# Kernel optimization log

Hardware: AMD Instinct MI355X
Metric: run time of the kernel (lower is better)

## Reference

```python
import jax, jax.numpy as jnp
import numpy as np

D_MODEL = 2048
N_HEADS = 16
HEAD_DIM = 128
WINDOW = 256
B, T = 2, 2048
SCALE = float(np.sqrt(HEAD_DIM))


def setup_inputs() -> dict:
    key = jax.random.key(0)
    ks = jax.random.split(key, 5)
    init = 0.02
    x = jax.random.normal(ks[0], (B, T, D_MODEL), dtype=jnp.float32)
    Wq = jax.random.normal(ks[1], (D_MODEL, D_MODEL), dtype=jnp.float32) * init
    Wk = jax.random.normal(ks[2], (D_MODEL, D_MODEL), dtype=jnp.float32) * init
    Wv = jax.random.normal(ks[3], (D_MODEL, D_MODEL), dtype=jnp.float32) * init
    Wo = jax.random.normal(ks[4], (D_MODEL, D_MODEL), dtype=jnp.float32) * init
    return {"x": x, "Wq": Wq, "Wk": Wk, "Wv": Wv, "Wo": Wo}


def _allowed_mask():
    # [H, T, T] bool: global (even) heads -> causal; local (odd) heads -> causal band of WINDOW
    idx = jnp.arange(T)
    causal = idx[None, :] <= idx[:, None]                      # [T, T]
    band = idx[None, :] >= (idx[:, None] - WINDOW + 1)         # [T, T]
    is_global = (jnp.arange(N_HEADS) % 2) == 0                 # [H]
    return causal[None] & (is_global[:, None, None] | band[None])


def reference(x, Wq, Wk, Wv, Wo):
    # projections (nn.Linear: y = x @ W.T), reshape to [B, H, T, D]
    def proj(W):
        return (x @ W.T).reshape(B, T, N_HEADS, HEAD_DIM).transpose(0, 2, 1, 3)

    q, k, v = proj(Wq), proj(Wk), proj(Wv)
    scores = jnp.einsum("bhtd,bhsd->bhts", q, k) / SCALE       # [B, H, T, T]
    allowed = _allowed_mask()                                  # [H, T, T]
    neg_inf = jnp.asarray(-jnp.inf, dtype=scores.dtype)
    scores = jnp.where(allowed[None], scores, neg_inf)
    attn = jax.nn.softmax(scores, axis=-1)
    out = jnp.einsum("bhts,bhsd->bhtd", attn, v)               # [B, H, T, D]
    concat = out.transpose(0, 2, 1, 3).reshape(B, T, N_HEADS * HEAD_DIM)
    return concat @ Wo.T
```

## Files before the change

kernel.cpp:

```cpp
#include <hip/hip_runtime.h>

typedef __attribute__((ext_vector_type(4))) float f32x4;
typedef __attribute__((ext_vector_type(8))) short bf16x8;
typedef __attribute__((ext_vector_type(4))) unsigned short u16x4;
typedef unsigned short u16;

#define MFMA16(a, b, c) __builtin_amdgcn_mfma_f32_16x16x32_bf16((a), (b), (c), 0, 0, 0)

#define T_SEQ 2048
#define DMODEL 2048
#define NHEADS 16
#define HDIM 128
#define WINDOW 256
#define MROWS 4096
#define SC 0.08838834764831845f

__device__ __forceinline__ u16 f2bf(float f) {
  union { float f; unsigned u; } v; v.f = f;
  return (u16)((v.u + 0x7FFFu + ((v.u >> 16) & 1u)) >> 16);
}
__device__ __forceinline__ float bf2f(u16 u) {
  union { unsigned u; float f; } v; v.u = ((unsigned)u) << 16;
  return v.f;
}
__device__ __forceinline__ void gl_lds16(const u16* g, u16* l) {
  __builtin_amdgcn_global_load_lds((const __attribute__((address_space(1))) void*)(g),
                                   (__attribute__((address_space(3))) void*)(l), 16, 0, 0);
}

#define BAR __builtin_amdgcn_s_barrier()
#define FEN asm volatile("" ::: "memory")
#define VMC3 asm volatile("s_waitcnt vmcnt(3)" ::: "memory")
#define VMC2 asm volatile("s_waitcnt vmcnt(2)" ::: "memory")
#define VMC0 asm volatile("s_waitcnt vmcnt(0)" ::: "memory")

__global__ __launch_bounds__(256) void convert_all(const float* __restrict__ x,
                                                   const float* __restrict__ wq,
                                                   const float* __restrict__ wk,
                                                   const float* __restrict__ wv,
                                                   const float* __restrict__ wo,
                                                   u16* __restrict__ dst) {
  const size_t NX = (size_t)MROWS * DMODEL;
  const size_t NW = (size_t)DMODEL * DMODEL;
  const size_t chunks = (NX + 4 * NW) / 8;
  for (size_t ci = (size_t)blockIdx.x * 256 + threadIdx.x; ci < chunks;
       ci += (size_t)gridDim.x * 256) {
    const size_t off = ci * 8;
    const float* src;
    size_t so;
    if (off < NX) { src = x; so = off; }
    else {
      size_t rem = off - NX;
      if (rem < NW) { src = wq; so = rem; }
      else if (rem < 2 * NW) { src = wk; so = rem - NW; }
      else if (rem < 3 * NW) { src = wv; so = rem - 2 * NW; }
      else { src = wo; so = rem - 3 * NW; }
    }
    f32x4 a = *(const f32x4*)&src[so];
    f32x4 b = *(const f32x4*)&src[so + 4];
    bf16x8 o;
#pragma unroll
    for (int j = 0; j < 4; ++j) { o[j] = (short)f2bf(a[j]); o[j + 4] = (short)f2bf(b[j]); }
    *(bf16x8*)&dst[off] = o;
  }
}

__global__ __launch_bounds__(512, 2) void gemm_qkv(const u16* __restrict__ A,
                                                   const u16* __restrict__ W,
                                                   u16* __restrict__ qb,
                                                   u16* __restrict__ kb,
                                                   u16* __restrict__ vb) {
  __shared__ u16 lds[57344];
  const int tid = threadIdx.x, w = tid >> 6, lane = tid & 63;
  const int wm = w >> 2, wn = w & 3;
  const int fr = lane & 15, g = lane >> 4, g4 = g * 4;

  const int xcd = blockIdx.x & 7, bi = blockIdx.x >> 3;
  const int mt = bi >> 2, nt = xcd * 4 + (bi & 3);
  const int m0 = mt * 256, n0 = nt * 192;

  const int xs0 = (g ^ (fr & 7)) * 8;
  const int xs1 = xs0 ^ 32;
  const int aRow = wm * 128 + fr;
  const int bRow = wn * 48 + fr;

  const int sr = tid >> 3;
  const int scc = ((tid & 7) ^ (sr & 7)) * 8;
  const u16* pA0  = A + (size_t)(m0 + sr) * DMODEL + scc;
  const u16* pA1  = A + (size_t)(m0 + 64 + sr) * DMODEL + scc;
  const u16* pB0  = W + (size_t)(n0 + sr) * DMODEL + scc;
  const u16* pB0b = W + (size_t)(n0 + 64 + sr) * DMODEL + scc;
  const u16* pB1  = W + (size_t)(n0 + 128 + sr) * DMODEL + scc;

#define SAH(h, t, c)                                                                   \
  { gl_lds16(pA0 + (size_t)(h) * 128 * DMODEL + (t) * 64,                              \
             &lds[(c) * 16384 + (h) * 8192 + w * 512]);                                \
    gl_lds16(pA1 + (size_t)(h) * 128 * DMODEL + (t) * 64,                              \
             &lds[(c) * 16384 + (h) * 8192 + 4096 + w * 512]); }
#define SBH0(t, c)                                                                     \
  { gl_lds16(pB0 + (size_t)(t) * 64, &lds[32768 + (c) * 12288 + w * 512]);             \
    gl_lds16(pB0b + (size_t)(t) * 64, &lds[32768 + (c) * 12288 + 4096 + w * 512]); }
#define SBH1(t, c)                                                                     \
  { gl_lds16(pB1 + (size_t)(t) * 64, &lds[32768 + (c) * 12288 + 8192 + w * 512]); }

#define RD_AL(c)                                                                       \
  { _Pragma("unroll") for (int m_ = 0; m_ < 4; ++m_) {                                 \
      af[m_][0] = *(const bf16x8*)&lds[(c) * 16384 + (aRow + m_ * 16) * 64 + xs0];     \
      af[m_][1] = *(const bf16x8*)&lds[(c) * 16384 + (aRow + m_ * 16) * 64 + xs1]; } }
#define RD_AH(c)                                                                       \
  { _Pragma("unroll") for (int m_ = 0; m_ < 4; ++m_) {                                 \
      af[m_][0] = *(const bf16x8*)&lds[(c) * 16384 + (aRow + 64 + m_ * 16) * 64 + xs0];\
      af[m_][1] = *(const bf16x8*)&lds[(c) * 16384 + (aRow + 64 + m_ * 16) * 64 + xs1]; } }
#define RD_B(c)                                                                        \
  { _Pragma("unroll") for (int n_ = 0; n_ < 3; ++n_) {                                 \
      bfr[n_][0] = *(const bf16x8*)&lds[32768 + (c) * 12288 + (bRow + n_ * 16) * 64 + xs0]; \
      bfr[n_][1] = *(const bf16x8*)&lds[32768 + (c) * 12288 + (bRow + n_ * 16) * 64 + xs1]; } }

#define MMQ(MB)                                                                        \
  { __builtin_amdgcn_s_setprio(1);                                                    \
    _Pragma("unroll") for (int kc_ = 0; kc_ < 2; ++kc_)                                \
      _Pragma("unroll") for (int m_ = 0; m_ < 4; ++m_)                                 \
        _Pragma("unroll") for (int n_ = 0; n_ < 3; ++n_)                               \
          acc[(MB) + m_][n_] = MFMA16(af[m_][kc_], bfr[n_][kc_], acc[(MB) + m_][n_]);  \
    __builtin_amdgcn_s_setprio(0); }

  bf16x8 af[4][2], bfr[3][2];
  f32x4 acc[8][3];
#pragma unroll
  for (int i = 0; i < 8; ++i)
#pragma unroll
    for (int j = 0; j < 3; ++j) acc[i][j] = (f32x4){0.f, 0.f, 0.f, 0.f};

  SAH(0, 0, 0); SAH(1, 0, 0);
  SBH0(0, 0); SBH1(0, 0);
  SBH0(1, 1); SBH1(1, 1);
  VMC3; BAR;

#pragma unroll 1
  for (int i = 0; i < 15; ++i) {
    const int t0 = 2 * i;
    RD_AL(0); RD_B(0); SAH(0, t0 + 1, 1); SAH(1, t0 + 1, 1);
    FEN; BAR; MMQ(0); FEN; BAR;
    RD_AH(0); SBH0(t0 + 2, 0); SBH1(t0 + 2, 0);
    VMC3; BAR; MMQ(4); FEN; BAR;
    RD_AL(1); RD_B(1); SAH(0, t0 + 2, 0); SAH(1, t0 + 2, 0);
    FEN; BAR; MMQ(0); FEN; BAR;
    RD_AH(1); SBH0(t0 + 3, 1); SBH1(t0 + 3, 1);
    VMC3; BAR; MMQ(4); FEN; BAR;
  }
  RD_AL(0); RD_B(0); SAH(0, 31, 1); SAH(1, 31, 1);
  FEN; BAR; MMQ(0); FEN; BAR;
  RD_AH(0);
  VMC0; BAR; MMQ(4); FEN; BAR;
  RD_AL(1); RD_B(1);
  FEN; BAR; MMQ(0); FEN; BAR;
  RD_AH(1);
  FEN; BAR; MMQ(4);

#pragma unroll
  for (int mi = 0; mi < 8; ++mi)
#pragma unroll
    for (int ni = 0; ni < 3; ++ni) {
      const int row0 = m0 + wm * 128 + mi * 16 + g4;
      const int cg = n0 + wn * 48 + ni * 16 + fr;
      const int bb = row0 >> 11, tl = row0 & 2047;
      if (cg < DMODEL) {
#pragma unroll
        for (int r = 0; r < 4; ++r)
          qb[(size_t)(row0 + r) * DMODEL + cg] = f2bf(acc[mi][ni][r] * SC);
      } else if (cg < 2 * DMODEL) {
        const int cc = cg - DMODEL;
        const int hh = cc >> 7, d = cc & 127;
        const size_t kbase = (size_t)(bb * NHEADS + hh) * T_SEQ * HDIM;
#pragma unroll
        for (int r = 0; r < 4; ++r)
          kb[kbase + (size_t)(tl + r) * HDIM + d] = f2bf(acc[mi][ni][r]);
      } else {
        const int cc = cg - 2 * DMODEL;
        const int hh = cc >> 7, d = cc & 127;
        u16x4 w4;
#pragma unroll
        for (int r = 0; r < 4; ++r) w4[r] = f2bf(acc[mi][ni][r]);
        *(u16x4*)&vb[(size_t)(bb * NHEADS + hh) * T_SEQ * HDIM + (size_t)(tl >> 6) * 8192 +
                     d * 64 + (tl & 63)] = w4;
      }
    }
#undef SAH
#undef SBH0
#undef SBH1
#undef RD_AL
#undef RD_AH
#undef RD_B
#undef MMQ
}

__global__ __launch_bounds__(512, 2) void gemm_out(const u16* __restrict__ A,
                                                   const u16* __restrict__ W0,
                                                   float* __restrict__ outf) {
  __shared__ u16 lds2[49152];
  const int tid = threadIdx.x, w = tid >> 6, lane = tid & 63;
  const int wm = w >> 2, wn = w & 3;
  const int fr = lane & 15, g = lane >> 4, g4 = g * 4;

  const int xcd = blockIdx.x & 7, bi = blockIdx.x >> 3;
  const int mt = bi >> 1, nt = xcd * 2 + (bi & 1);
  const int m0 = mt * 256, n0 = nt * 128;

  const int xs0 = (g ^ (fr & 7)) * 8;
  const int xs1 = xs0 ^ 32;
  const int aRow = wm * 128 + fr;
  const int bRow = wn * 32 + fr;

  const int sr = tid >> 3;
  const int scc = ((tid & 7) ^ (sr & 7)) * 8;
  const u16* pA0  = A + (size_t)(m0 + sr) * DMODEL + scc;
  const u16* pA1  = A + (size_t)(m0 + 64 + sr) * DMODEL + scc;
  const u16* pB0  = W0 + (size_t)(n0 + sr) * DMODEL + scc;
  const u16* pB0b = W0 + (size_t)(n0 + 64 + sr) * DMODEL + scc;

#define S2A(h, t, c)                                                                   \
  { gl_lds16(pA0 + (size_t)(h) * 128 * DMODEL + (t) * 64,                              \
             &lds2[(c) * 16384 + (h) * 8192 + w * 512]);                               \
    gl_lds16(pA1 + (size_t)(h) * 128 * DMODEL + (t) * 64,                              \
             &lds2[(c) * 16384 + (h) * 8192 + 4096 + w * 512]); }
#define S2B(t, c)                                                                      \
  { gl_lds16(pB0 + (size_t)(t) * 64, &lds2[32768 + (c) * 8192 + w * 512]);             \
    gl_lds16(pB0b + (size_t)(t) * 64, &lds2[32768 + (c) * 8192 + 4096 + w * 512]); }

#define R2AL(c)                                                                        \
  { _Pragma("unroll") for (int m_ = 0; m_ < 4; ++m_) {                                 \
      af[m_][0] = *(const bf16x8*)&lds2[(c) * 16384 + (aRow + m_ * 16) * 64 + xs0];    \
      af[m_][1] = *(const bf16x8*)&lds2[(c) * 16384 + (aRow + m_ * 16) * 64 + xs1]; } }
#define R2AH(c)                                                                        \
  { _Pragma("unroll") for (int m_ = 0; m_ < 4; ++m_) {                                 \
      af[m_][0] = *(const bf16x8*)&lds2[(c) * 16384 + (aRow + 64 + m_ * 16) * 64 + xs0]; \
      af[m_][1] = *(const bf16x8*)&lds2[(c) * 16384 + (aRow + 64 + m_ * 16) * 64 + xs1]; } }
#define R2B(c)                                                                         \
  { _Pragma("unroll") for (int n_ = 0; n_ < 2; ++n_) {                                 \
      bfr[n_][0] = *(const bf16x8*)&lds2[32768 + (c) * 8192 + (bRow + n_ * 16) * 64 + xs0]; \
      bfr[n_][1] = *(const bf16x8*)&lds2[32768 + (c) * 8192 + (bRow + n_ * 16) * 64 + xs1]; } }

#define M2(MB)                                                                         \
  { __builtin_amdgcn_s_setprio(1);                                                    \
    _Pragma("unroll") for (int kc_ = 0; kc_ < 2; ++kc_)                                \
      _Pragma("unroll") for (int m_ = 0; m_ < 4; ++m_)                                 \
        _Pragma("unroll") for (int n_ = 0; n_ < 2; ++n_)                               \
          acc[(MB) + m_][n_] = MFMA16(af[m_][kc_], bfr[n_][kc_], acc[(MB) + m_][n_]);  \
    __builtin_amdgcn_s_setprio(0); }

  bf16x8 af[4][2], bfr[2][2];
  f32x4 acc[8][2];
#pragma unroll
  for (int i = 0; i < 8; ++i)
#pragma unroll
    for (int j = 0; j < 2; ++j) acc[i][j] = (f32x4){0.f, 0.f, 0.f, 0.f};

  S2A(0, 0, 0); S2A(1, 0, 0);
  S2B(0, 0);
  S2B(1, 1);
  VMC2; BAR;

#pragma unroll 1
  for (int i = 0; i < 15; ++i) {
    const int t0 = 2 * i;
    R2AL(0); R2B(0); S2A(0, t0 + 1, 1); S2A(1, t0 + 1, 1);
    FEN; BAR; M2(0); FEN; BAR;
    R2AH(0); S2B(t0 + 2, 0);
    VMC2; BAR; M2(4); FEN; BAR;
    R2AL(1); R2B(1); S2A(0, t0 + 2, 0); S2A(1, t0 + 2, 0);
    FEN; BAR; M2(0); FEN; BAR;
    R2AH(1); S2B(t0 + 3, 1);
    VMC2; BAR; M2(4); FEN; BAR;
  }
  R2AL(0); R2B(0); S2A(0, 31, 1); S2A(1, 31, 1);
  FEN; BAR; M2(0); FEN; BAR;
  R2AH(0);
  VMC0; BAR; M2(4); FEN; BAR;
  R2AL(1); R2B(1);
  FEN; BAR; M2(0); FEN; BAR;
  R2AH(1);
  FEN; BAR; M2(4);

#pragma unroll
  for (int mi = 0; mi < 8; ++mi)
#pragma unroll
    for (int ni = 0; ni < 2; ++ni) {
      const int row0 = m0 + wm * 128 + mi * 16 + g4;
      const int c = n0 + wn * 32 + ni * 16 + fr;
#pragma unroll
      for (int r = 0; r < 4; ++r)
        outf[(size_t)(row0 + r) * DMODEL + c] = acc[mi][ni][r];
    }
#undef S2A
#undef S2B
#undef R2AL
#undef R2AH
#undef R2B
#undef M2
}

#define QB 128
#define KVB 64

__global__ __launch_bounds__(512, 4) void attn_kernel(const u16* __restrict__ qb,
                                                      const u16* __restrict__ kb,
                                                      const u16* __restrict__ vb,
                                                      u16* __restrict__ op,
                                                      u16* __restrict__ pO,
                                                      float* __restrict__ pm,
                                                      float* __restrict__ pl) {
  __shared__ u16 lds[40960];

  const int xcdid = blockIdx.x & 7, j = blockIdx.x >> 3;
  const int p = xcdid * 4 + j / 24;
  const int bx = j % 24;
  const int h = p & 15, b = p >> 4;

  const bool isglobal = (h & 1) == 0;
  int qt, klo, khi, part = 0;
  bool partial = false;
  if (isglobal) {
    if (bx < 16) {
      qt = 15 - (bx >> 1);
      part = bx & 1;
      partial = true;
      if (part == 0) { klo = 0; khi = 15; } else { klo = 16; khi = 2 * qt + 1; }
    } else {
      qt = 23 - bx;
      klo = 0; khi = 2 * qt + 1;
    }
  } else {
    if (bx >= 16) return;
    qt = 15 - bx;
    const int lo_ = qt * QB - (WINDOW - 1);
    klo = lo_ > 0 ? (lo_ >> 6) : 0;
    khi = 2 * qt + 1;
  }

  const int tid = threadIdx.x, wave = tid >> 6, lane = tid & 63;
  const int fr = lane & 15, g = lane >> 4, g4 = g * 4;
  const int xk = fr & 7;
  const int q0 = qt * QB;
  const int bh = b * NHEADS + h;
  const size_t basek = (size_t)bh * T_SEQ * HDIM;
  const size_t baseo = (size_t)b * T_SEQ * DMODEL + (size_t)h * HDIM;

  bf16x8 qf[4];
  {
    const int qrow = q0 + wave * 16 + fr;
#pragma unroll
    for (int ds = 0; ds < 4; ++ds)
      qf[ds] = *(const bf16x8*)&qb[(size_t)b * T_SEQ * DMODEL + (size_t)qrow * DMODEL +
                                   (size_t)h * HDIM + ds * 32 + g * 8];
  }

  float mrun = -1e30f, lrun = 0.f;
  f32x4 o[8];
#pragma unroll
  for (int dt = 0; dt < 8; ++dt) o[dt] = (f32x4){0.f, 0.f, 0.f, 0.f};

  const int j0 = wave * 2, j1 = wave * 2 + 1;
  const int gi0 = j0 * 64 + lane, gi1 = j1 * 64 + lane;
  const int kr0 = gi0 >> 4, kc0 = (gi0 & 15) ^ (kr0 & 7);
  const int kr1 = gi1 >> 4, kc1 = (gi1 & 15) ^ (kr1 & 7);
  const u16* pK0 = kb + basek + (size_t)kr0 * HDIM + kc0 * 8;
  const u16* pK1 = kb + basek + (size_t)kr1 * HDIM + kc1 * 8;
  const int d0 = gi0 >> 3, vs0 = (gi0 & 7) ^ (d0 & 7);
  const int d1 = gi1 >> 3, vs1 = (gi1 & 7) ^ (d1 & 7);
  const u16* pV0 = vb + basek + (size_t)d0 * 64 + vs0 * 8;
  const u16* pV1 = vb + basek + (size_t)d1 * 64 + vs1 * 8;

#define STAGE(KT, c)                                                                   \
  { gl_lds16(pK0 + (size_t)(KT) * 8192, &lds[(c) * 8192 + j0 * 512]);                  \
    gl_lds16(pK1 + (size_t)(KT) * 8192, &lds[(c) * 8192 + j1 * 512]);                  \
    gl_lds16(pV0 + (size_t)(KT) * 8192, &lds[16384 + (c) * 8192 + j0 * 512]);          \
    gl_lds16(pV1 + (size_t)(KT) * 8192, &lds[16384 + (c) * 8192 + j1 * 512]); }

  u16* Pw = &lds[32768 + wave * 1024];
  const int qg = q0 + wave * 16 + fr;

  STAGE(klo, klo & 1);
  VMC0; BAR;

  for (int kt = klo; kt <= khi; ++kt) {
    const int c = kt & 1;
    const bool more = kt < khi;
    if (more) STAGE(kt + 1, c ^ 1);
    const u16* Kc = &lds[c * 8192];
    const u16* Vc = &lds[16384 + c * 8192];

    f32x4 s[4];
    __builtin_amdgcn_s_setprio(1);
#pragma unroll
    for (int kk = 0; kk < 4; ++kk) {
      f32x4 a = (f32x4){0.f, 0.f, 0.f, 0.f};
#pragma unroll
      for (int ds = 0; ds < 4; ++ds) {
        const int r = kk * 16 + fr;
        bf16x8 kf = *(const bf16x8*)&Kc[r * 128 + (((ds * 4 + g) ^ xk) << 3)];
        a = MFMA16(kf, qf[ds], a);
      }
      s[kk] = a;
    }
    __builtin_amdgcn_s_setprio(0);

    float sv[16];
    float pmax = -1e30f;
#pragma unroll
    for (int kk = 0; kk < 4; ++kk)
#pragma unroll
      for (int reg = 0; reg < 4; ++reg) {
        const int cg = kt * KVB + kk * 16 + g4 + reg;
        const bool allowed = (cg <= qg) && (isglobal || cg >= qg - (WINDOW - 1));
        const float v = allowed ? s[kk][reg] : -1e30f;
        sv[kk * 4 + reg] = v;
        pmax = fmaxf(pmax, v);
      }
    pmax = fmaxf(pmax, __shfl_xor(pmax, 16, 64));
    pmax = fmaxf(pmax, __shfl_xor(pmax, 32, 64));
    const bool resc = !__all(pmax - mrun <= 8.0f);
    float fac = 1.f;
    if (resc) {
      const float nm = fmaxf(mrun, pmax);
      fac = __expf(mrun - nm);
      mrun = nm;
    }
    float rs = 0.f;
    u16 pb[16];
#pragma unroll
    for (int i = 0; i < 16; ++i) {
      const float p_ = (sv[i] > -5e29f) ? __expf(sv[i] - mrun) : 0.f;
      rs += p_;
      pb[i] = f2bf(p_);
    }
    rs += __shfl_xor(rs, 16, 64);
    rs += __shfl_xor(rs, 32, 64);
    lrun = lrun * fac + rs;

#pragma unroll
    for (int kk = 0; kk < 4; ++kk) {
      u16x4 wv;
      wv[0] = pb[kk * 4]; wv[1] = pb[kk * 4 + 1]; wv[2] = pb[kk * 4 + 2]; wv[3] = pb[kk * 4 + 3];
      *(u16x4*)&Pw[fr * 64 + (((2 * kk + (g >> 1)) ^ xk) << 3) + (g & 1) * 4] = wv;
    }

    if (resc) {
      float ff[4];
#pragma unroll
      for (int r = 0; r < 4; ++r) ff[r] = __shfl(fac, g4 + r, 64);
#pragma unroll
      for (int dt = 0; dt < 8; ++dt)
#pragma unroll
        for (int r = 0; r < 4; ++r) o[dt][r] *= ff[r];
    }

    bf16x8 pf0 = *(const bf16x8*)&Pw[fr * 64 + ((g ^ xk) << 3)];
    bf16x8 pf1 = *(const bf16x8*)&Pw[fr * 64 + (((4 + g) ^ xk) << 3)];
    __builtin_amdgcn_s_setprio(1);
#pragma unroll
    for (int dt = 0; dt < 8; ++dt) {
      const int d = dt * 16 + fr;
      bf16x8 vf0 = *(const bf16x8*)&Vc[d * 64 + ((g ^ xk) << 3)];
      bf16x8 vf1 = *(const bf16x8*)&Vc[d * 64 + (((4 + g) ^ xk) << 3)];
      o[dt] = MFMA16(pf0, vf0, o[dt]);
      o[dt] = MFMA16(pf1, vf1, o[dt]);
    }
    __builtin_amdgcn_s_setprio(0);

    FEN;
    VMC0;
    BAR;
  }

  if (!partial) {
    const float inv = 1.0f / lrun;
    float iv[4];
#pragma unroll
    for (int r = 0; r < 4; ++r) iv[r] = __shfl(inv, g4 + r, 64);
#pragma unroll
    for (int r = 0; r < 4; ++r) {
      const int qrow = q0 + wave * 16 + g4 + r;
#pragma unroll
      for (int dt = 0; dt < 8; ++dt)
        op[baseo + (size_t)qrow * DMODEL + dt * 16 + fr] = f2bf(o[dt][r] * iv[r]);
    }
  } else {
    const int sidx = (((b * 8 + (h >> 1)) * 8 + (qt - 8)) << 1) + part;
    const size_t sb = (size_t)sidx * QB;
#pragma unroll
    for (int r = 0; r < 4; ++r) {
      const size_t row = sb + wave * 16 + g4 + r;
#pragma unroll
      for (int dt = 0; dt < 8; ++dt)
        pO[row * HDIM + dt * 16 + fr] = f2bf(o[dt][r]);
    }
    if (lane < 16) {
      pm[sb + wave * 16 + lane] = mrun;
      pl[sb + wave * 16 + lane] = lrun;
    }
  }
#undef STAGE
}

__global__ __launch_bounds__(256) void merge_kernel(const u16* __restrict__ pO,
                                                    const float* __restrict__ pm,
                                                    const float* __restrict__ pl,
                                                    u16* __restrict__ op) {
  const int x = blockIdx.x;
  const int qt8 = x & 7, eh = (x >> 3) & 7, b = x >> 6;
  const int h = eh * 2, qt = 8 + qt8;
  const int s0 = x * 2, s1 = s0 + 1;

  for (int i = 0; i < 8; ++i) {
    const int vidx = threadIdx.x + i * 256;
    const int row = vidx >> 4, d8 = (vidx & 15) * 8;
    const float m0 = pm[s0 * QB + row], m1 = pm[s1 * QB + row];
    const float l0 = pl[s0 * QB + row], l1 = pl[s1 * QB + row];
    const float m = fmaxf(m0, m1);
    const float w0 = __expf(m0 - m), w1 = __expf(m1 - m);
    const float inv = 1.0f / (l0 * w0 + l1 * w1);
    bf16x8 a = *(const bf16x8*)&pO[((size_t)s0 * QB + row) * HDIM + d8];
    bf16x8 c = *(const bf16x8*)&pO[((size_t)s1 * QB + row) * HDIM + d8];
    bf16x8 r;
#pragma unroll
    for (int j = 0; j < 8; ++j)
      r[j] = (short)f2bf((bf2f((u16)a[j]) * w0 + bf2f((u16)c[j]) * w1) * inv);
    *(bf16x8*)&op[((size_t)(b * T_SEQ + qt * QB + row)) * DMODEL + h * HDIM + d8] = r;
  }
}

extern "C" void kernel_launch(void* const* d_in, const int* in_sizes, int n_in,
                              void* d_out, int out_size, void* d_ws, size_t ws_size,
                              hipStream_t stream) {
  (void)in_sizes; (void)n_in; (void)out_size; (void)ws_size;
  const float* x  = (const float*)d_in[0];
  const float* Wq = (const float*)d_in[1];
  const float* Wk = (const float*)d_in[2];
  const float* Wv = (const float*)d_in[3];
  const float* Wo = (const float*)d_in[4];

  const size_t NX = (size_t)MROWS * DMODEL;
  const size_t NW = (size_t)DMODEL * DMODEL;
  u16* ws  = (u16*)d_ws;
  u16* xb  = ws;
  u16* wqb = ws + NX;
  u16* wkb = wqb + NW;
  u16* wvb = wkb + NW;
  u16* wob = wvb + NW;
  u16* qbb = wob + NW;
  u16* kbb = qbb + NX;
  u16* vbb = kbb + NX;

  u16*   pO = wqb;
  float* pm = (float*)(wqb + (size_t)256 * QB * HDIM);
  float* pl = pm + 256 * QB;

  convert_all<<<2048, 256, 0, stream>>>(x, Wq, Wk, Wv, Wo, ws);

  gemm_qkv<<<512, 512, 0, stream>>>(xb, wqb, qbb, kbb, vbb);

  attn_kernel<<<768, 512, 0, stream>>>(qbb, kbb, vbb, xb, pO, pm, pl);

  merge_kernel<<<128, 256, 0, stream>>>(pO, pm, pl, xb);

  gemm_out<<<256, 512, 0, stream>>>(xb, wob, (float*)d_out);
}
```

Before: 216.0 us.

## Halve GEMM block M-tile to 128 with 4 waves, doubling grid size

Both projection GEMMs move from 512-thread blocks with 256-row tiles (2x4 waves) to 256-thread blocks with 128-row tiles (1x4 waves). The grids double and LDS per block shrinks, and the staging loads and vmcnt thresholds are rewritten to match. The aim is better occupancy and load balance across CUs. In exchange, each block reuses its B tile across fewer rows, which raises total global and LDS traffic for the weight operand.

```diff
diff --git a/kernel.cpp b/kernel.cpp
--- a/kernel.cpp
+++ b/kernel.cpp
@@ -30,8 +30,8 @@
 
 #define BAR __builtin_amdgcn_s_barrier()
 #define FEN asm volatile("" ::: "memory")
-#define VMC3 asm volatile("s_waitcnt vmcnt(3)" ::: "memory")
-#define VMC2 asm volatile("s_waitcnt vmcnt(2)" ::: "memory")
+#define VMC6 asm volatile("s_waitcnt vmcnt(6)" ::: "memory")
+#define VMC4 asm volatile("s_waitcnt vmcnt(4)" ::: "memory")
 #define VMC0 asm volatile("s_waitcnt vmcnt(0)" ::: "memory")
 
 __global__ __launch_bounds__(256) void convert_all(const float* __restrict__ x,
@@ -65,56 +65,56 @@
   }
 }
 
-__global__ __launch_bounds__(512, 2) void gemm_qkv(const u16* __restrict__ A,
+__global__ __launch_bounds__(256, 2) void gemm_qkv(const u16* __restrict__ A,
                                                    const u16* __restrict__ W,
                                                    u16* __restrict__ qb,
                                                    u16* __restrict__ kb,
                                                    u16* __restrict__ vb) {
-  __shared__ u16 lds[57344];
+  __shared__ u16 lds[40960];
   const int tid = threadIdx.x, w = tid >> 6, lane = tid & 63;
-  const int wm = w >> 2, wn = w & 3;
   const int fr = lane & 15, g = lane >> 4, g4 = g * 4;
+  const int xk = fr & 7;
 
   const int xcd = blockIdx.x & 7, bi = blockIdx.x >> 3;
   const int mt = bi >> 2, nt = xcd * 4 + (bi & 3);
-  const int m0 = mt * 256, n0 = nt * 192;
-
-  const int xs0 = (g ^ (fr & 7)) * 8;
+  const int m0 = mt * 128, n0 = nt * 192;
+
+  const int xs0 = (g ^ xk) * 8;
   const int xs1 = xs0 ^ 32;
-  const int aRow = wm * 128 + fr;
-  const int bRow = wn * 48 + fr;
-
-  const int sr = tid >> 3;
-  const int scc = ((tid & 7) ^ (sr & 7)) * 8;
-  const u16* pA0  = A + (size_t)(m0 + sr) * DMODEL + scc;
-  const u16* pA1  = A + (size_t)(m0 + 64 + sr) * DMODEL + scc;
-  const u16* pB0  = W + (size_t)(n0 + sr) * DMODEL + scc;
-  const u16* pB0b = W + (size_t)(n0 + 64 + sr) * DMODEL + scc;
-  const u16* pB1  = W + (size_t)(n0 + 128 + sr) * DMODEL + scc;
-
-#define SAH(h, t, c)                                                                   \
-  { gl_lds16(pA0 + (size_t)(h) * 128 * DMODEL + (t) * 64,                              \
-             &lds[(c) * 16384 + (h) * 8192 + w * 512]);                                \
-    gl_lds16(pA1 + (size_t)(h) * 128 * DMODEL + (t) * 64,                              \
-             &lds[(c) * 16384 + (h) * 8192 + 4096 + w * 512]); }
-#define SBH0(t, c)                                                                     \
-  { gl_lds16(pB0 + (size_t)(t) * 64, &lds[32768 + (c) * 12288 + w * 512]);             \
-    gl_lds16(pB0b + (size_t)(t) * 64, &lds[32768 + (c) * 12288 + 4096 + w * 512]); }
-#define SBH1(t, c)                                                                     \
-  { gl_lds16(pB1 + (size_t)(t) * 64, &lds[32768 + (c) * 12288 + 8192 + w * 512]); }
+  const int bRow = w * 48 + fr;
+
+  const u16* pA[4];
+  const u16* pB[6];
+#pragma unroll
+  for (int j = 0; j < 4; ++j) {
+    const int gi = j * 256 + tid, row = gi >> 3, ch = (gi & 7) ^ (row & 7);
+    pA[j] = A + (size_t)(m0 + row) * DMODEL + ch * 8;
+  }
+#pragma unroll
+  for (int j = 0; j < 6; ++j) {
+    const int gi = j * 256 + tid, row = gi >> 3, ch = (gi & 7) ^ (row & 7);
+    pB[j] = W + (size_t)(n0 + row) * DMODEL + ch * 8;
+  }
+
+#define SA(t, c)                                                                       \
+  { _Pragma("unroll") for (int j = 0; j < 4; ++j)                                      \
+      gl_lds16(pA[j] + (size_t)(t) * 64, &lds[(c) * 8192 + j * 2048 + w * 512]); }
+#define SB(t, c)                                                                       \
+  { _Pragma("unroll") for (int j = 0; j < 6; ++j)                                      \
+      gl_lds16(pB[j] + (size_t)(t) * 64, &lds[16384 + (c) * 12288 + j * 2048 + w * 512]); }
 
 #define RD_AL(c)                                                                       \
   { _Pragma("unroll") for (int m_ = 0; m_ < 4; ++m_) {                                 \
-      af[m_][0] = *(const bf16x8*)&lds[(c) * 16384 + (aRow + m_ * 16) * 64 + xs0];     \
-      af[m_][1] = *(const bf16x8*)&lds[(c) * 16384 + (aRow + m_ * 16) * 64 + xs1]; } }
+      af[m_][0] = *(const bf16x8*)&lds[(c) * 8192 + (fr + m_ * 16) * 64 + xs0];        \
+      af[m_][1] = *(const bf16x8*)&lds[(c) * 8192 + (fr + m_ * 16) * 64 + xs1]; } }
 #define RD_AH(c)                                                                       \
   { _Pragma("unroll") for (int m_ = 0; m_ < 4; ++m_) {                                 \
-      af[m_][0] = *(const bf16x8*)&lds[(c) * 16384 + (aRow + 64 + m_ * 16) * 64 + xs0];\
-      af[m_][1] = *(const bf16x8*)&lds[(c) * 16384 + (aRow + 64 + m_ * 16) * 64 + xs1]; } }
+      af[m_][0] = *(const bf16x8*)&lds[(c) * 8192 + (fr + 64 + m_ * 16) * 64 + xs0];   \
+      af[m_][1] = *(const bf16x8*)&lds[(c) * 8192 + (fr + 64 + m_ * 16) * 64 + xs1]; } }
 #define RD_B(c)                                                                        \
   { _Pragma("unroll") for (int n_ = 0; n_ < 3; ++n_) {                                 \
-      bfr[n_][0] = *(const bf16x8*)&lds[32768 + (c) * 12288 + (bRow + n_ * 16) * 64 + xs0]; \
-      bfr[n_][1] = *(const bf16x8*)&lds[32768 + (c) * 12288 + (bRow + n_ * 16) * 64 + xs1]; } }
+      bfr[n_][0] = *(const bf16x8*)&lds[16384 + (c) * 12288 + (bRow + n_ * 16) * 64 + xs0]; \
+      bfr[n_][1] = *(const bf16x8*)&lds[16384 + (c) * 12288 + (bRow + n_ * 16) * 64 + xs1]; } }
 
 #define MMQ(MB)                                                                        \
   { __builtin_amdgcn_s_setprio(1);                                                    \
@@ -131,24 +131,23 @@
 #pragma unroll
     for (int j = 0; j < 3; ++j) acc[i][j] = (f32x4){0.f, 0.f, 0.f, 0.f};
 
-  SAH(0, 0, 0); SAH(1, 0, 0);
-  SBH0(0, 0); SBH1(0, 0);
-  SBH0(1, 1); SBH1(1, 1);
-  VMC3; BAR;
+  SA(0, 0); SB(0, 0);
+  SB(1, 1);
+  VMC6; BAR;
 
 #pragma unroll 1
   for (int i = 0; i < 15; ++i) {
     const int t0 = 2 * i;
-    RD_AL(0); RD_B(0); SAH(0, t0 + 1, 1); SAH(1, t0 + 1, 1);
+    RD_AL(0); RD_B(0); SA(t0 + 1, 1);
     FEN; BAR; MMQ(0); FEN; BAR;
-    RD_AH(0); SBH0(t0 + 2, 0); SBH1(t0 + 2, 0);
-    VMC3; BAR; MMQ(4); FEN; BAR;
-    RD_AL(1); RD_B(1); SAH(0, t0 + 2, 0); SAH(1, t0 + 2, 0);
+    RD_AH(0); SB(t0 + 2, 0);
+    VMC6; BAR; MMQ(4); FEN; BAR;
+    RD_AL(1); RD_B(1); SA(t0 + 2, 0);
     FEN; BAR; MMQ(0); FEN; BAR;
-    RD_AH(1); SBH0(t0 + 3, 1); SBH1(t0 + 3, 1);
-    VMC3; BAR; MMQ(4); FEN; BAR;
-  }
-  RD_AL(0); RD_B(0); SAH(0, 31, 1); SAH(1, 31, 1);
+    RD_AH(1); SB(t0 + 3, 1);
+    VMC6; BAR; MMQ(4); FEN; BAR;
+  }
+  RD_AL(0); RD_B(0); SA(31, 1);
   FEN; BAR; MMQ(0); FEN; BAR;
   RD_AH(0);
   VMC0; BAR; MMQ(4); FEN; BAR;
@@ -161,8 +160,8 @@
   for (int mi = 0; mi < 8; ++mi)
 #pragma unroll
     for (int ni = 0; ni < 3; ++ni) {
-      const int row0 = m0 + wm * 128 + mi * 16 + g4;
-      const int cg = n0 + wn * 48 + ni * 16 + fr;
+      const int row0 = m0 + mi * 16 + g4;
+      const int cg = n0 + w * 48 + ni * 16 + fr;
       const int bb = row0 >> 11, tl = row0 & 2047;
       if (cg < DMODEL) {
 #pragma unroll
@@ -185,60 +184,58 @@
                      d * 64 + (tl & 63)] = w4;
       }
     }
-#undef SAH
-#undef SBH0
-#undef SBH1
+#undef SA
+#undef SB
 #undef RD_AL
 #undef RD_AH
 #undef RD_B
 #undef MMQ
 }
 
-__global__ __launch_bounds__(512, 2) void gemm_out(const u16* __restrict__ A,
+__global__ __launch_bounds__(256, 2) void gemm_out(const u16* __restrict__ A,
                                                    const u16* __restrict__ W0,
                                                    float* __restrict__ outf) {
-  __shared__ u16 lds2[49152];
+  __shared__ u16 lds2[32768];
   const int tid = threadIdx.x, w = tid >> 6, lane = tid & 63;
-  const int wm = w >> 2, wn = w & 3;
   const int fr = lane & 15, g = lane >> 4, g4 = g * 4;
+  const int xk = fr & 7;
 
   const int xcd = blockIdx.x & 7, bi = blockIdx.x >> 3;
   const int mt = bi >> 1, nt = xcd * 2 + (bi & 1);
-  const int m0 = mt * 256, n0 = nt * 128;
-
-  const int xs0 = (g ^ (fr & 7)) * 8;
+  const int m0 = mt * 128, n0 = nt * 128;
+
+  const int xs0 = (g ^ xk) * 8;
   const int xs1 = xs0 ^ 32;
-  const int aRow = wm * 128 + fr;
-  const int bRow = wn * 32 + fr;
-
-  const int sr = tid >> 3;
-  const int scc = ((tid & 7) ^ (sr & 7)) * 8;
-  const u16* pA0  = A + (size_t)(m0 + sr) * DMODEL + scc;
-  const u16* pA1  = A + (size_t)(m0 + 64 + sr) * DMODEL + scc;
-  const u16* pB0  = W0 + (size_t)(n0 + sr) * DMODEL + scc;
-  const u16* pB0b = W0 + (size_t)(n0 + 64 + sr) * DMODEL + scc;
-
-#define S2A(h, t, c)                                                                   \
-  { gl_lds16(pA0 + (size_t)(h) * 128 * DMODEL + (t) * 64,                              \
-             &lds2[(c) * 16384 + (h) * 8192 + w * 512]);                               \
-    gl_lds16(pA1 + (size_t)(h) * 128 * DMODEL + (t) * 64,                              \
-             &lds2[(c) * 16384 + (h) * 8192 + 4096 + w * 512]); }
+  const int bRow = w * 32 + fr;
+
+  const u16* pA[4];
+  const u16* pB[4];
+#pragma unroll
+  for (int j = 0; j < 4; ++j) {
+    const int gi = j * 256 + tid, row = gi >> 3, ch = (gi & 7) ^ (row & 7);
+    pA[j] = A + (size_t)(m0 + row) * DMODEL + ch * 8;
+    pB[j] = W0 + (size_t)(n0 + row) * DMODEL + ch * 8;
+  }
+
+#define S2A(t, c)                                                                      \
+  { _Pragma("unroll") for (int j = 0; j < 4; ++j)                                      \
+      gl_lds16(pA[j] + (size_t)(t) * 64, &lds2[(c) * 8192 + j * 2048 + w * 512]); }
 #define S2B(t, c)                                                                      \
-  { gl_lds16(pB0 + (size_t)(t) * 64, &lds2[32768 + (c) * 8192 + w * 512]);             \
-    gl_lds16(pB0b + (size_t)(t) * 64, &lds2[32768 + (c) * 8192 + 4096 + w * 512]); }
+  { _Pragma("unroll") for (int j = 0; j < 4; ++j)                                      \
+      gl_lds16(pB[j] + (size_t)(t) * 64, &lds2[16384 + (c) * 8192 + j * 2048 + w * 512]); }
 
 #define R2AL(c)                                                                        \
   { _Pragma("unroll") for (int m_ = 0; m_ < 4; ++m_) {                                 \
-      af[m_][0] = *(const bf16x8*)&lds2[(c) * 16384 + (aRow + m_ * 16) * 64 + xs0];    \
-      af[m_][1] = *(const bf16x8*)&lds2[(c) * 16384 + (aRow + m_ * 16) * 64 + xs1]; } }
+      af[m_][0] = *(const bf16x8*)&lds2[(c) * 8192 + (fr + m_ * 16) * 64 + xs0];       \
+      af[m_][1] = *(const bf16x8*)&lds2[(c) * 8192 + (fr + m_ * 16) * 64 + xs1]; } }
 #define R2AH(c)                                                                        \
   { _Pragma("unroll") for (int m_ = 0; m_ < 4; ++m_) {                                 \
-      af[m_][0] = *(const bf16x8*)&lds2[(c) * 16384 + (aRow + 64 + m_ * 16) * 64 + xs0]; \
-      af[m_][1] = *(const bf16x8*)&lds2[(c) * 16384 + (aRow + 64 + m_ * 16) * 64 + xs1]; } }
+      af[m_][0] = *(const bf16x8*)&lds2[(c) * 8192 + (fr + 64 + m_ * 16) * 64 + xs0];  \
+      af[m_][1] = *(const bf16x8*)&lds2[(c) * 8192 + (fr + 64 + m_ * 16) * 64 + xs1]; } }
 #define R2B(c)                                                                         \
   { _Pragma("unroll") for (int n_ = 0; n_ < 2; ++n_) {                                 \
-      bfr[n_][0] = *(const bf16x8*)&lds2[32768 + (c) * 8192 + (bRow + n_ * 16) * 64 + xs0]; \
-      bfr[n_][1] = *(const bf16x8*)&lds2[32768 + (c) * 8192 + (bRow + n_ * 16) * 64 + xs1]; } }
+      bfr[n_][0] = *(const bf16x8*)&lds2[16384 + (c) * 8192 + (bRow + n_ * 16) * 64 + xs0]; \
+      bfr[n_][1] = *(const bf16x8*)&lds2[16384 + (c) * 8192 + (bRow + n_ * 16) * 64 + xs1]; } }
 
 #define M2(MB)                                                                         \
   { __builtin_amdgcn_s_setprio(1);                                                    \
@@ -255,24 +252,23 @@
 #pragma unroll
     for (int j = 0; j < 2; ++j) acc[i][j] = (f32x4){0.f, 0.f, 0.f, 0.f};
 
-  S2A(0, 0, 0); S2A(1, 0, 0);
-  S2B(0, 0);
+  S2A(0, 0); S2B(0, 0);
   S2B(1, 1);
-  VMC2; BAR;
+  VMC4; BAR;
 
 #pragma unroll 1
   for (int i = 0; i < 15; ++i) {
     const int t0 = 2 * i;
-    R2AL(0); R2B(0); S2A(0, t0 + 1, 1); S2A(1, t0 + 1, 1);
+    R2AL(0); R2B(0); S2A(t0 + 1, 1);
     FEN; BAR; M2(0); FEN; BAR;
     R2AH(0); S2B(t0 + 2, 0);
-    VMC2; BAR; M2(4); FEN; BAR;
-    R2AL(1); R2B(1); S2A(0, t0 + 2, 0); S2A(1, t0 + 2, 0);
+    VMC4; BAR; M2(4); FEN; BAR;
+    R2AL(1); R2B(1); S2A(t0 + 2, 0);
     FEN; BAR; M2(0); FEN; BAR;
     R2AH(1); S2B(t0 + 3, 1);
-    VMC2; BAR; M2(4); FEN; BAR;
-  }
-  R2AL(0); R2B(0); S2A(0, 31, 1); S2A(1, 31, 1);
+    VMC4; BAR; M2(4); FEN; BAR;
+  }
+  R2AL(0); R2B(0); S2A(31, 1);
   FEN; BAR; M2(0); FEN; BAR;
   R2AH(0);
   VMC0; BAR; M2(4); FEN; BAR;
@@ -285,8 +281,8 @@
   for (int mi = 0; mi < 8; ++mi)
 #pragma unroll
     for (int ni = 0; ni < 2; ++ni) {
-      const int row0 = m0 + wm * 128 + mi * 16 + g4;
-      const int c = n0 + wn * 32 + ni * 16 + fr;
+      const int row0 = m0 + mi * 16 + g4;
+      const int c = n0 + w * 32 + ni * 16 + fr;
 #pragma unroll
       for (int r = 0; r < 4; ++r)
         outf[(size_t)(row0 + r) * DMODEL + c] = acc[mi][ni][r];
@@ -557,11 +553,11 @@
 
   convert_all<<<2048, 256, 0, stream>>>(x, Wq, Wk, Wv, Wo, ws);
 
-  gemm_qkv<<<512, 512, 0, stream>>>(xb, wqb, qbb, kbb, vbb);
+  gemm_qkv<<<1024, 256, 0, stream>>>(xb, wqb, qbb, kbb, vbb);
 
   attn_kernel<<<768, 512, 0, stream>>>(qbb, kbb, vbb, xb, pO, pm, pl);
 
   merge_kernel<<<128, 256, 0, stream>>>(pO, pm, pl, xb);
 
-  gemm_out<<<256, 512, 0, stream>>>(xb, wob, (float*)d_out);
-}
+  gemm_out<<<512, 256, 0, stream>>>(xb, wob, (float*)d_out);
+}
```

New measurement: 211.0 us (median of 2 runs). 1.02x faster.
